# Optimization experiments

Hardware: AMD Instinct MI355X
Metric: run time of the kernel (lower is better)

The kernel has to match this reference:

```python
import jax, jax.numpy as jnp
import numpy as np

EPS = 1e-5

def conv(x, w, stride=1, pad=0):
    # x: NCHW, w: OIHW
    return jax.lax.conv_general_dilated(
        x, w, (stride, stride), [(pad, pad), (pad, pad)],
        dimension_numbers=('NCHW', 'OIHW', 'NCHW'))

def bn(x, g, b, m, v):
    scale = (g * jax.lax.rsqrt(v + EPS))[None, :, None, None]
    shift = (b - m * g * jax.lax.rsqrt(v + EPS))[None, :, None, None]
    return x * scale + shift

def dilate3x3(mask):
    # binary dilation == 3x3 max-pool, stride 1, pad 1
    return jax.lax.reduce_window(mask, -jnp.inf, jax.lax.max,
                                 (1, 1, 3, 3), (1, 1, 1, 1),
                                 [(0, 0), (0, 0), (1, 1), (1, 1)])

def setup_inputs() -> dict:
    key = jax.random.key(0)
    ks = jax.random.split(key, 8)
    B, Cin, H, W = 32, 256, 56, 56
    width, Cout = 64, 256
    f32 = jnp.float32
    return {
        'x':       jax.random.normal(ks[0], (B, Cin, H, W), f32),
        'conv1_w': jax.random.normal(ks[1], (width, Cin, 1, 1), f32) * 0.05,
        'conv2_w': jax.random.normal(ks[2], (width, width, 3, 3), f32) * 0.05,
        'conv3_w': jax.random.normal(ks[3], (Cout, width, 1, 1), f32) * 0.05,
        'bn1_g': jnp.ones((width,), f32), 'bn1_b': jnp.zeros((width,), f32),
        'bn1_m': jax.random.normal(ks[4], (width,), f32) * 0.1,
        'bn1_v': jax.random.uniform(ks[4], (width,), f32, 0.5, 1.5),
        'bn2_g': jnp.ones((width,), f32), 'bn2_b': jnp.zeros((width,), f32),
        'bn2_m': jax.random.normal(ks[5], (width,), f32) * 0.1,
        'bn2_v': jax.random.uniform(ks[5], (width,), f32, 0.5, 1.5),
        'bn3_g': jnp.ones((Cout,), f32), 'bn3_b': jnp.zeros((Cout,), f32),
        'bn3_m': jax.random.normal(ks[6], (Cout,), f32) * 0.1,
        'bn3_v': jax.random.uniform(ks[6], (Cout,), f32, 0.5, 1.5),
        'mask_w': jax.random.normal(ks[7], (1, Cin, 1, 1), f32) * 0.05,
        'mask_b': jnp.zeros((1,), f32),
    }

def reference(x, conv1_w, conv2_w, conv3_w,
              bn1_g, bn1_b, bn1_m, bn1_v,
              bn2_g, bn2_b, bn2_m, bn2_v,
              bn3_g, bn3_b, bn3_m, bn3_v,
              mask_w, mask_b):
    identity = x  # stride=1, no downsample
    # --- MaskUnit: 1x1 conv squeeze -> hard binary mask (inference Gumbel) ---
    soft = conv(x, mask_w) + mask_b[None, :, None, None]   # [B,1,H,W]
    mask = (soft >= 0.0).astype(x.dtype)                    # 'std' mask
    mask_dilate = dilate3x3(mask)                           # 'dilate' mask
    # --- sparse bottleneck: compute only on active positions (zero elsewhere) ---
    h = conv(x, conv1_w)                                    # [B,64,H,W]
    h = jax.nn.relu(bn(h, bn1_g, bn1_b, bn1_m, bn1_v)) * mask_dilate
    h = conv(h, conv2_w, stride=1, pad=1)
    h = jax.nn.relu(bn(h, bn2_g, bn2_b, bn2_m, bn2_v)) * mask
    h = conv(h, conv3_w)                                    # [B,256,H,W]
    h = bn(h, bn3_g, bn3_b, bn3_m, bn3_v) * mask            # apply_mask
    out = jax.nn.relu(identity + h)
    return out
```

## Files before the change

kernel.cpp:

```cpp
#include <hip/hip_runtime.h>
#include <hip/hip_bf16.h>


#define BATCH 32
#define CIN   256
#define WIDTH 64
#define COUT  256
#define HH    56
#define WW    56
#define HW    3136
#define EPS   1e-5f
#define XSTR  40
#define H1ROW 7424

typedef __attribute__((ext_vector_type(8))) short bf16x8;
typedef __attribute__((ext_vector_type(4))) float f32x4;

static __device__ __forceinline__ unsigned short f2bf(float f) {
    __hip_bfloat16 h = __float2bfloat16(f);
    return *reinterpret_cast<unsigned short*>(&h);
}

__global__ __launch_bounds__(384) void kbn(
    const float* __restrict__ g1, const float* __restrict__ b1,
    const float* __restrict__ m1, const float* __restrict__ v1,
    const float* __restrict__ g2, const float* __restrict__ b2,
    const float* __restrict__ m2, const float* __restrict__ v2,
    const float* __restrict__ g3, const float* __restrict__ b3,
    const float* __restrict__ m3, const float* __restrict__ v3,
    float* __restrict__ tabs)
{
    int t = threadIdx.x;
    if (t < 64) {
        float sc = g1[t] * rsqrtf(v1[t] + EPS);
        tabs[t] = sc; tabs[64 + t] = b1[t] - m1[t] * sc;
    } else if (t < 128) {
        int o = t - 64;
        float sc = g2[o] * rsqrtf(v2[o] + EPS);
        tabs[128 + o] = sc; tabs[192 + o] = b2[o] - m2[o] * sc;
    } else if (t < 384) {
        int o = t - 128;
        float sc = g3[o] * rsqrtf(v3[o] + EPS);
        tabs[256 + o] = sc; tabs[512 + o] = b3[o] - m3[o] * sc;
    }
}

__global__ __launch_bounds__(256) void kw_pack(
    const float* __restrict__ w1, const float* __restrict__ w2,
    const float* __restrict__ w3, __hip_bfloat16* __restrict__ w1p,
    __hip_bfloat16* __restrict__ w2p, __hip_bfloat16* __restrict__ w3q)
{
    int idx = blockIdx.x * 256 + threadIdx.x;
    if (idx < 16384) {
        int j = idx & 7, l = (idx >> 3) & 63;
        int mt = (idx >> 9) & 3, kt = idx >> 11;
        int o = mt * 16 + (l & 15);
        int c = kt * 32 + (l >> 4) * 8 + j;
        *reinterpret_cast<unsigned short*>(w1p + idx) = f2bf(w1[o * CIN + c]);
    } else if (idx < 16384 + 36864) {
        int i2 = idx - 16384;
        int j = i2 & 7, l = (i2 >> 3) & 63;
        int mt = (i2 >> 9) & 3, kt = (i2 >> 11) & 1, tap = i2 >> 12;
        int o = mt * 16 + (l & 15);
        int c = kt * 32 + (l >> 4) * 8 + j;
        *reinterpret_cast<unsigned short*>(w2p + i2) =
            f2bf(w2[(o * WIDTH + c) * 9 + tap]);
    } else if (idx < 16384 + 36864 + 16384) {
        int i3 = idx - 16384 - 36864;
        int j = i3 & 7, l = (i3 >> 3) & 63;
        int ot = (i3 >> 9) & 15, kt = i3 >> 13;
        int oc = ot * 16 + (l & 15);
        int c = kt * 32 + (l >> 4) * 8 + j;
        *reinterpret_cast<unsigned short*>(w3q + i3) = f2bf(w3[oc * WIDTH + c]);
    }
}

__global__ __launch_bounds__(256) void k1_mfma(
    const float* __restrict__ x, const __hip_bfloat16* __restrict__ w1p,
    const float* __restrict__ sc1, const float* __restrict__ sh1,
    const float* __restrict__ mw, const float* __restrict__ mb,
    __hip_bfloat16* __restrict__ h1g, float* __restrict__ mask)
{
    __shared__ __align__(16) unsigned short xs[2][64 * XSTR];
    __shared__ __align__(16) float mtab[16][68];

    const int tid = threadIdx.x;
    const int l = tid & 63, w = tid >> 6;
    const int ln = l & 15, lg = l >> 4;
    const int b = blockIdx.y;
    const int px0 = blockIdx.x * 64;
    const float* __restrict__ xb = x + (size_t)b * CIN * HW;
    const bf16x8* __restrict__ w1v = reinterpret_cast<const bf16x8*>(w1p);

    const int chA = tid >> 4;
    const int pxs = (tid & 15) * 4;
    float msum[4] = {0.f, 0.f, 0.f, 0.f};

    auto STAGE = [&](int kt, int bufi) {
        const float* xp = xb + (size_t)(kt * 32 + chA) * HW + px0 + pxs;
        float4 va = *reinterpret_cast<const float4*>(xp);
        float4 vb = *reinterpret_cast<const float4*>(xp + (size_t)16 * HW);
        float mwa = mw[kt * 32 + chA], mwb = mw[kt * 32 + 16 + chA];
        msum[0] += va.x * mwa + vb.x * mwb;
        msum[1] += va.y * mwa + vb.y * mwb;
        msum[2] += va.z * mwa + vb.z * mwb;
        msum[3] += va.w * mwa + vb.w * mwb;
        unsigned base = (unsigned)pxs * XSTR + chA;
        xs[bufi][base + 0 * XSTR] = f2bf(va.x);
        xs[bufi][base + 1 * XSTR] = f2bf(va.y);
        xs[bufi][base + 2 * XSTR] = f2bf(va.z);
        xs[bufi][base + 3 * XSTR] = f2bf(va.w);
        xs[bufi][base + 16 + 0 * XSTR] = f2bf(vb.x);
        xs[bufi][base + 16 + 1 * XSTR] = f2bf(vb.y);
        xs[bufi][base + 16 + 2 * XSTR] = f2bf(vb.z);
        xs[bufi][base + 16 + 3 * XSTR] = f2bf(vb.w);
    };

    f32x4 acc[4];
    #pragma unroll
    for (int m = 0; m < 4; ++m) acc[m] = f32x4{0.f, 0.f, 0.f, 0.f};

    STAGE(0, 0);
    __syncthreads();

    const unsigned fidx = (unsigned)(w * 16 + ln) * XSTR + lg * 8;
    #pragma unroll
    for (int kt = 0; kt < 8; ++kt) {
        const int cur = kt & 1;
        if (kt < 7) STAGE(kt + 1, cur ^ 1);
        bf16x8 bfr = *reinterpret_cast<const bf16x8*>(&xs[cur][fidx]);
        #pragma unroll
        for (int mt = 0; mt < 4; ++mt) {
            bf16x8 a = w1v[(kt * 4 + mt) * 64 + l];
            acc[mt] = __builtin_amdgcn_mfma_f32_16x16x32_bf16(a, bfr, acc[mt], 0, 0, 0);
        }
        __syncthreads();
    }

    *reinterpret_cast<float4*>(&mtab[chA][pxs]) =
        make_float4(msum[0], msum[1], msum[2], msum[3]);
    __syncthreads();
    if (tid < 64) {
        float s = 0.f;
        #pragma unroll
        for (int g = 0; g < 16; ++g) s += mtab[g][tid];
        mask[b * HW + px0 + tid] = (s + mb[0] >= 0.f) ? 1.f : 0.f;
    }

    const int p = px0 + w * 16 + ln;
    const int y = p / 56, xcn = p - y * 56;
    const int pxp = xcn + 1;
    const unsigned key = (unsigned)(pxp & 7) << 3;
    const size_t rowbase = (((size_t)b * 58 + y + 1) * 58 + pxp) * 64;
    #pragma unroll
    for (int mt = 0; mt < 4; ++mt) {
        int ob = mt * 16 + lg * 4;
        ushort4 u;
        u.x = f2bf(fmaxf(acc[mt][0] * sc1[ob + 0] + sh1[ob + 0], 0.f));
        u.y = f2bf(fmaxf(acc[mt][1] * sc1[ob + 1] + sh1[ob + 1], 0.f));
        u.z = f2bf(fmaxf(acc[mt][2] * sc1[ob + 2] + sh1[ob + 2], 0.f));
        u.w = f2bf(fmaxf(acc[mt][3] * sc1[ob + 3] + sh1[ob + 3], 0.f));
        *reinterpret_cast<ushort4*>(h1g + rowbase + (ob ^ key)) = u;
    }
}

__global__ __launch_bounds__(256) void k1b_dilate(
    const float* __restrict__ mask, __hip_bfloat16* __restrict__ h1g)
{
    int idx = blockIdx.x * 256 + threadIdx.x;
    if (idx >= BATCH * 58 * 58) return;
    int b   = idx / 3364;
    int rem = idx - b * 3364;
    int r = rem / 58, c = rem - r * 58;

    bool zero;
    if (r == 0 || r == 57 || c == 0 || c == 57) {
        zero = true;
    } else {
        int y = r - 1, x = c - 1;
        float mx = 0.f;
        #pragma unroll
        for (int dy = -1; dy <= 1; ++dy)
            #pragma unroll
            for (int dx = -1; dx <= 1; ++dx) {
                int yy = y + dy, xx = x + dx;
                if (yy >= 0 && yy < HH && xx >= 0 && xx < WW)
                    mx = fmaxf(mx, mask[b * HW + yy * WW + xx]);
            }
        zero = (mx < 0.5f);
    }
    if (zero) {
        uint4 z = make_uint4(0u, 0u, 0u, 0u);
        uint4* p = reinterpret_cast<uint4*>(h1g + (size_t)idx * 64);
        #pragma unroll
        for (int k = 0; k < 8; ++k) p[k] = z;
    }
}

__global__ __launch_bounds__(256) void k2_mfma(
    const __hip_bfloat16* __restrict__ h1g,
    const __hip_bfloat16* __restrict__ w2p,
    const float* __restrict__ sc2, const float* __restrict__ sh2,
    const float* __restrict__ mask, __hip_bfloat16* __restrict__ h2)
{
    __shared__ __align__(16) char smem[30720];

    const int tid = threadIdx.x;
    const int l = tid & 63, w = tid >> 6;
    const int b = blockIdx.y;
    const int yr0 = blockIdx.x * 2;
    const int yrow = yr0 + (w & 1);
    const int mh = w >> 1;
    const int ln = l & 15, lg = l >> 4;

    {
        const char* src = (const char*)h1g + ((size_t)b * 58 + yr0) * H1ROW;
        #pragma unroll
        for (int t = 0; t < 8; ++t) {
            int c = t * 4 + w;
            if (c < 29) {
                __builtin_amdgcn_global_load_lds(
                    (const __attribute__((address_space(1))) void*)(src + c * 1024 + l * 16),
                    (__attribute__((address_space(3))) void*)(smem + c * 1024),
                    16, 0, 0);
            }
        }
    }

    const bf16x8* __restrict__ w2v = reinterpret_cast<const bf16x8*>(w2p);

    f32x4 acc[2][4];
    #pragma unroll
    for (int i = 0; i < 2; ++i)
        #pragma unroll
        for (int j = 0; j < 4; ++j) acc[i][j] = f32x4{0.f, 0.f, 0.f, 0.f};

    __syncthreads();

    #pragma unroll
    for (int dy = 0; dy < 3; ++dy) {
        const int lr = (w & 1) + dy;
        #pragma unroll
        for (int dx = 0; dx < 3; ++dx) {
            const int tap = dy * 3 + dx;
            #pragma unroll
            for (int kt = 0; kt < 2; ++kt) {
                bf16x8 a0 = w2v[((tap * 2 + kt) * 4 + mh * 2 + 0) * 64 + l];
                bf16x8 a1 = w2v[((tap * 2 + kt) * 4 + mh * 2 + 1) * 64 + l];
                bf16x8 bf[4];
                #pragma unroll
                for (int nt = 0; nt < 4; ++nt) {
                    int colp = nt * 16 + ln + dx;
                    unsigned off = (unsigned)lr * H1ROW + (unsigned)colp * 128
                                 + (((unsigned)(kt * 64 + lg * 16))
                                    ^ (((unsigned)colp & 7u) << 4));
                    bf[nt] = *reinterpret_cast<const bf16x8*>(smem + off);
                }
                #pragma unroll
                for (int nt = 0; nt < 4; ++nt) {
                    acc[0][nt] = __builtin_amdgcn_mfma_f32_16x16x32_bf16(
                        a0, bf[nt], acc[0][nt], 0, 0, 0);
                    acc[1][nt] = __builtin_amdgcn_mfma_f32_16x16x32_bf16(
                        a1, bf[nt], acc[1][nt], 0, 0, 0);
                }
            }
        }
    }

    #pragma unroll
    for (int nt = 0; nt < 4; ++nt) {
        int xc = nt * 16 + ln;
        if (xc < WW) {
            int p = yrow * WW + xc;
            float mkv = mask[b * HW + p];
            #pragma unroll
            for (int mi = 0; mi < 2; ++mi) {
                int ob = (mh * 2 + mi) * 16 + lg * 4;
                ushort4 u;
                u.x = f2bf(fmaxf(acc[mi][nt][0] * sc2[ob + 0] + sh2[ob + 0], 0.f) * mkv);
                u.y = f2bf(fmaxf(acc[mi][nt][1] * sc2[ob + 1] + sh2[ob + 1], 0.f) * mkv);
                u.z = f2bf(fmaxf(acc[mi][nt][2] * sc2[ob + 2] + sh2[ob + 2], 0.f) * mkv);
                u.w = f2bf(fmaxf(acc[mi][nt][3] * sc2[ob + 3] + sh2[ob + 3], 0.f) * mkv);
                *reinterpret_cast<ushort4*>(h2 + ((size_t)b * HW + p) * 64 + ob) = u;
            }
        }
    }
}

__global__ __launch_bounds__(256) void k3_mfma(
    const __hip_bfloat16* __restrict__ h2, const __hip_bfloat16* __restrict__ w3q,
    const float* __restrict__ sc3, const float* __restrict__ sh3,
    const float* __restrict__ x, const float* __restrict__ mask,
    float* __restrict__ out)
{
    const int tid = threadIdx.x;
    const int l = tid & 63, w = tid >> 6;
    const int ln = l & 15, lg = l >> 4;
    const int b = blockIdx.y;
    const int yr = blockIdx.x;

    const bf16x8* __restrict__ h2v = reinterpret_cast<const bf16x8*>(h2)
                                   + ((size_t)b * HW + yr * WW) * 8;
    const bf16x8* __restrict__ w3v = reinterpret_cast<const bf16x8*>(w3q);

    float4 mk4[4];
    #pragma unroll
    for (int pt = 0; pt < 4; ++pt) {
        int pxb = pt * 16 + lg * 4;
        mk4[pt] = (pxb < WW)
            ? *reinterpret_cast<const float4*>(&mask[(size_t)b * HW + yr * WW + pxb])
            : make_float4(0.f, 0.f, 0.f, 0.f);
    }
    float4 xv[4][4];
    #pragma unroll
    for (int ot = 0; ot < 4; ++ot) {
        const int oc = w * 64 + ot * 16 + ln;
        const size_t rbase = ((size_t)b * COUT + oc) * HW + yr * WW;
        #pragma unroll
        for (int pt = 0; pt < 4; ++pt) {
            int pxb = pt * 16 + lg * 4;
            if (pxb < WW)
                xv[ot][pt] = *reinterpret_cast<const float4*>(&x[rbase + pxb]);
        }
    }

    f32x4 acc[4][4];
    #pragma unroll
    for (int p = 0; p < 4; ++p)
        #pragma unroll
        for (int o = 0; o < 4; ++o) acc[p][o] = f32x4{0.f, 0.f, 0.f, 0.f};

    #pragma unroll
    for (int kt = 0; kt < 2; ++kt) {
        bf16x8 af[4];
        #pragma unroll
        for (int pt = 0; pt < 4; ++pt)
            af[pt] = h2v[(pt * 16 + ln) * 8 + kt * 4 + lg];
        #pragma unroll
        for (int ot = 0; ot < 4; ++ot) {
            bf16x8 bw = w3v[(kt * 16 + w * 4 + ot) * 64 + l];
            #pragma unroll
            for (int pt = 0; pt < 4; ++pt)
                acc[pt][ot] = __builtin_amdgcn_mfma_f32_16x16x32_bf16(
                    af[pt], bw, acc[pt][ot], 0, 0, 0);
        }
    }

    #pragma unroll
    for (int ot = 0; ot < 4; ++ot) {
        const int oc = w * 64 + ot * 16 + ln;
        const float sc = sc3[oc], sh = sh3[oc];
        const size_t rbase = ((size_t)b * COUT + oc) * HW + yr * WW;
        #pragma unroll
        for (int pt = 0; pt < 4; ++pt) {
            int pxb = pt * 16 + lg * 4;
            if (pxb < WW) {
                float4 o4;
                o4.x = fmaxf(xv[ot][pt].x + (acc[pt][ot][0] * sc + sh) * mk4[pt].x, 0.f);
                o4.y = fmaxf(xv[ot][pt].y + (acc[pt][ot][1] * sc + sh) * mk4[pt].y, 0.f);
                o4.z = fmaxf(xv[ot][pt].z + (acc[pt][ot][2] * sc + sh) * mk4[pt].z, 0.f);
                o4.w = fmaxf(xv[ot][pt].w + (acc[pt][ot][3] * sc + sh) * mk4[pt].w, 0.f);
                *reinterpret_cast<float4*>(&out[rbase + pxb]) = o4;
            }
        }
    }
}

extern "C" void kernel_launch(void* const* d_in, const int* in_sizes, int n_in,
                              void* d_out, int out_size, void* d_ws, size_t ws_size,
                              hipStream_t stream)
{
    const float* x  = (const float*)d_in[0];
    const float* w1 = (const float*)d_in[1];
    const float* w2 = (const float*)d_in[2];
    const float* w3 = (const float*)d_in[3];
    const float* g1 = (const float*)d_in[4];
    const float* b1 = (const float*)d_in[5];
    const float* m1 = (const float*)d_in[6];
    const float* v1 = (const float*)d_in[7];
    const float* g2 = (const float*)d_in[8];
    const float* b2 = (const float*)d_in[9];
    const float* m2 = (const float*)d_in[10];
    const float* v2 = (const float*)d_in[11];
    const float* g3 = (const float*)d_in[12];
    const float* b3 = (const float*)d_in[13];
    const float* m3 = (const float*)d_in[14];
    const float* v3 = (const float*)d_in[15];
    const float* mw = (const float*)d_in[16];
    const float* mb = (const float*)d_in[17];
    float* outp = (float*)d_out;

    char* p = (char*)d_ws;
    __hip_bfloat16* h1g = (__hip_bfloat16*)p;  p += (size_t)BATCH * 3364 * 64 * 2;
    __hip_bfloat16* h2  = (__hip_bfloat16*)p;  p += (size_t)BATCH * HW * 64 * 2;
    float* mask = (float*)p;                   p += (size_t)BATCH * HW * 4;
    __hip_bfloat16* w1p = (__hip_bfloat16*)p;  p += 16384 * 2;
    __hip_bfloat16* w2p = (__hip_bfloat16*)p;  p += 36864 * 2;
    __hip_bfloat16* w3q = (__hip_bfloat16*)p;  p += 16384 * 2;
    float* tabs = (float*)p;
    float* sc1 = tabs;       float* sh1 = tabs + 64;
    float* sc2 = tabs + 128; float* sh2 = tabs + 192;
    float* sc3 = tabs + 256; float* sh3 = tabs + 512;

    kbn<<<dim3(1), dim3(384), 0, stream>>>(g1, b1, m1, v1, g2, b2, m2, v2,
                                           g3, b3, m3, v3, tabs);
    kw_pack<<<dim3(272), dim3(256), 0, stream>>>(w1, w2, w3, w1p, w2p, w3q);

    k1_mfma<<<dim3(49, BATCH), dim3(256), 0, stream>>>(x, w1p, sc1, sh1, mw, mb,
                                                       h1g, mask);

    int npad = BATCH * 3364;
    k1b_dilate<<<dim3((npad + 255) / 256), dim3(256), 0, stream>>>(mask, h1g);

    k2_mfma<<<dim3(HH / 2, BATCH), dim3(256), 0, stream>>>(h1g, w2p, sc2, sh2,
                                                           mask, h2);

    k3_mfma<<<dim3(HH, BATCH), dim3(256), 0, stream>>>(h2, w3q, sc3, sh3,
                                                       x, mask, outp);
}
```

Before: 102.1 us.

## Fuse dilated-mask zeroing into conv2 smem tile, merge BN prep, split conv3 channels

The separate dilation kernel, which zeroed inactive and border positions of h1 in global memory, is removed. Instead, k2 computes the 3x3 max of the mask for each staged pixel and zeroes those pixels directly in its shared-memory tile after the async load. The BN-table kernel is folded into the weight-packing kernel as an extra block, saving one launch. k3 now splits output channels across a new grid z dimension of 2 to raise parallelism and cut per-thread accumulators, at the cost of reading h2 twice.

```diff
diff --git a/kernel.cpp b/kernel.cpp
--- a/kernel.cpp
+++ b/kernel.cpp
@@ -21,7 +21,10 @@
     return *reinterpret_cast<unsigned short*>(&h);
 }
 
-__global__ __launch_bounds__(384) void kbn(
+__global__ __launch_bounds__(256) void kw_pack(
+    const float* __restrict__ w1, const float* __restrict__ w2,
+    const float* __restrict__ w3, __hip_bfloat16* __restrict__ w1p,
+    __hip_bfloat16* __restrict__ w2p, __hip_bfloat16* __restrict__ w3q,
     const float* __restrict__ g1, const float* __restrict__ b1,
     const float* __restrict__ m1, const float* __restrict__ v1,
     const float* __restrict__ g2, const float* __restrict__ b2,
@@ -30,26 +33,23 @@
     const float* __restrict__ m3, const float* __restrict__ v3,
     float* __restrict__ tabs)
 {
-    int t = threadIdx.x;
-    if (t < 64) {
-        float sc = g1[t] * rsqrtf(v1[t] + EPS);
-        tabs[t] = sc; tabs[64 + t] = b1[t] - m1[t] * sc;
-    } else if (t < 128) {
-        int o = t - 64;
-        float sc = g2[o] * rsqrtf(v2[o] + EPS);
-        tabs[128 + o] = sc; tabs[192 + o] = b2[o] - m2[o] * sc;
-    } else if (t < 384) {
-        int o = t - 128;
-        float sc = g3[o] * rsqrtf(v3[o] + EPS);
-        tabs[256 + o] = sc; tabs[512 + o] = b3[o] - m3[o] * sc;
-    }
-}
-
-__global__ __launch_bounds__(256) void kw_pack(
-    const float* __restrict__ w1, const float* __restrict__ w2,
-    const float* __restrict__ w3, __hip_bfloat16* __restrict__ w1p,
-    __hip_bfloat16* __restrict__ w2p, __hip_bfloat16* __restrict__ w3q)
-{
+    if (blockIdx.x == 272) {
+        for (int t = threadIdx.x; t < 384; t += 256) {
+            if (t < 64) {
+                float sc = g1[t] * rsqrtf(v1[t] + EPS);
+                tabs[t] = sc; tabs[64 + t] = b1[t] - m1[t] * sc;
+            } else if (t < 128) {
+                int o = t - 64;
+                float sc = g2[o] * rsqrtf(v2[o] + EPS);
+                tabs[128 + o] = sc; tabs[192 + o] = b2[o] - m2[o] * sc;
+            } else {
+                int o = t - 128;
+                float sc = g3[o] * rsqrtf(v3[o] + EPS);
+                tabs[256 + o] = sc; tabs[512 + o] = b3[o] - m3[o] * sc;
+            }
+        }
+        return;
+    }
     int idx = blockIdx.x * 256 + threadIdx.x;
     if (idx < 16384) {
         int j = idx & 7, l = (idx >> 3) & 63;
@@ -164,39 +164,6 @@
     }
 }
 
-__global__ __launch_bounds__(256) void k1b_dilate(
-    const float* __restrict__ mask, __hip_bfloat16* __restrict__ h1g)
-{
-    int idx = blockIdx.x * 256 + threadIdx.x;
-    if (idx >= BATCH * 58 * 58) return;
-    int b   = idx / 3364;
-    int rem = idx - b * 3364;
-    int r = rem / 58, c = rem - r * 58;
-
-    bool zero;
-    if (r == 0 || r == 57 || c == 0 || c == 57) {
-        zero = true;
-    } else {
-        int y = r - 1, x = c - 1;
-        float mx = 0.f;
-        #pragma unroll
-        for (int dy = -1; dy <= 1; ++dy)
-            #pragma unroll
-            for (int dx = -1; dx <= 1; ++dx) {
-                int yy = y + dy, xx = x + dx;
-                if (yy >= 0 && yy < HH && xx >= 0 && xx < WW)
-                    mx = fmaxf(mx, mask[b * HW + yy * WW + xx]);
-            }
-        zero = (mx < 0.5f);
-    }
-    if (zero) {
-        uint4 z = make_uint4(0u, 0u, 0u, 0u);
-        uint4* p = reinterpret_cast<uint4*>(h1g + (size_t)idx * 64);
-        #pragma unroll
-        for (int k = 0; k < 8; ++k) p[k] = z;
-    }
-}
-
 __global__ __launch_bounds__(256) void k2_mfma(
     const __hip_bfloat16* __restrict__ h1g,
     const __hip_bfloat16* __restrict__ w2p,
@@ -235,6 +202,35 @@
         #pragma unroll
         for (int j = 0; j < 4; ++j) acc[i][j] = f32x4{0.f, 0.f, 0.f, 0.f};
 
+    __syncthreads();
+
+    if (tid < 232) {
+        const int pr = tid / 58;
+        const int pc = tid - pr * 58;
+        const int gr = yr0 + pr;
+        bool zero;
+        if (gr == 0 || gr == 57 || pc == 0 || pc == 57) {
+            zero = true;
+        } else {
+            const int y = gr - 1, xc = pc - 1;
+            float mx = 0.f;
+            #pragma unroll
+            for (int dy = -1; dy <= 1; ++dy)
+                #pragma unroll
+                for (int dx = -1; dx <= 1; ++dx) {
+                    int yy = y + dy, xx = xc + dx;
+                    if (yy >= 0 && yy < HH && xx >= 0 && xx < WW)
+                        mx = fmaxf(mx, mask[b * HW + yy * WW + xx]);
+                }
+            zero = (mx < 0.5f);
+        }
+        if (zero) {
+            uint4* q = reinterpret_cast<uint4*>(smem + pr * H1ROW + pc * 128);
+            uint4 zz = make_uint4(0u, 0u, 0u, 0u);
+            #pragma unroll
+            for (int k = 0; k < 8; ++k) q[k] = zz;
+        }
+    }
     __syncthreads();
 
     #pragma unroll
@@ -298,6 +294,7 @@
     const int ln = l & 15, lg = l >> 4;
     const int b = blockIdx.y;
     const int yr = blockIdx.x;
+    const int z = blockIdx.z;
 
     const bf16x8* __restrict__ h2v = reinterpret_cast<const bf16x8*>(h2)
                                    + ((size_t)b * HW + yr * WW) * 8;
@@ -311,10 +308,10 @@
             ? *reinterpret_cast<const float4*>(&mask[(size_t)b * HW + yr * WW + pxb])
             : make_float4(0.f, 0.f, 0.f, 0.f);
     }
-    float4 xv[4][4];
-    #pragma unroll
-    for (int ot = 0; ot < 4; ++ot) {
-        const int oc = w * 64 + ot * 16 + ln;
+    float4 xv[2][4];
+    #pragma unroll
+    for (int ot = 0; ot < 2; ++ot) {
+        const int oc = w * 64 + z * 32 + ot * 16 + ln;
         const size_t rbase = ((size_t)b * COUT + oc) * HW + yr * WW;
         #pragma unroll
         for (int pt = 0; pt < 4; ++pt) {
@@ -324,11 +321,11 @@
         }
     }
 
-    f32x4 acc[4][4];
+    f32x4 acc[4][2];
     #pragma unroll
     for (int p = 0; p < 4; ++p)
         #pragma unroll
-        for (int o = 0; o < 4; ++o) acc[p][o] = f32x4{0.f, 0.f, 0.f, 0.f};
+        for (int o = 0; o < 2; ++o) acc[p][o] = f32x4{0.f, 0.f, 0.f, 0.f};
 
     #pragma unroll
     for (int kt = 0; kt < 2; ++kt) {
@@ -337,8 +334,8 @@
         for (int pt = 0; pt < 4; ++pt)
             af[pt] = h2v[(pt * 16 + ln) * 8 + kt * 4 + lg];
         #pragma unroll
-        for (int ot = 0; ot < 4; ++ot) {
-            bf16x8 bw = w3v[(kt * 16 + w * 4 + ot) * 64 + l];
+        for (int ot = 0; ot < 2; ++ot) {
+            bf16x8 bw = w3v[(kt * 16 + w * 4 + z * 2 + ot) * 64 + l];
             #pragma unroll
             for (int pt = 0; pt < 4; ++pt)
                 acc[pt][ot] = __builtin_amdgcn_mfma_f32_16x16x32_bf16(
@@ -347,8 +344,8 @@
     }
 
     #pragma unroll
-    for (int ot = 0; ot < 4; ++ot) {
-        const int oc = w * 64 + ot * 16 + ln;
+    for (int ot = 0; ot < 2; ++ot) {
+        const int oc = w * 64 + z * 32 + ot * 16 + ln;
         const float sc = sc3[oc], sh = sh3[oc];
         const size_t rbase = ((size_t)b * COUT + oc) * HW + yr * WW;
         #pragma unroll
@@ -402,19 +399,16 @@
     float* sc2 = tabs + 128; float* sh2 = tabs + 192;
     float* sc3 = tabs + 256; float* sh3 = tabs + 512;
 
-    kbn<<<dim3(1), dim3(384), 0, stream>>>(g1, b1, m1, v1, g2, b2, m2, v2,
-                                           g3, b3, m3, v3, tabs);
-    kw_pack<<<dim3(272), dim3(256), 0, stream>>>(w1, w2, w3, w1p, w2p, w3q);
+    kw_pack<<<dim3(273), dim3(256), 0, stream>>>(w1, w2, w3, w1p, w2p, w3q,
+                                                 g1, b1, m1, v1, g2, b2, m2, v2,
+                                                 g3, b3, m3, v3, tabs);
 
     k1_mfma<<<dim3(49, BATCH), dim3(256), 0, stream>>>(x, w1p, sc1, sh1, mw, mb,
                                                        h1g, mask);
 
-    int npad = BATCH * 3364;
-    k1b_dilate<<<dim3((npad + 255) / 256), dim3(256), 0, stream>>>(mask, h1g);
-
     k2_mfma<<<dim3(HH / 2, BATCH), dim3(256), 0, stream>>>(h1g, w2p, sc2, sh2,
                                                            mask, h2);
 
-    k3_mfma<<<dim3(HH, BATCH), dim3(256), 0, stream>>>(h2, w3q, sc3, sh3,
-                                                       x, mask, outp);
-}
+    k3_mfma<<<dim3(HH, BATCH, 2), dim3(256), 0, stream>>>(h2, w3q, sc3, sh3,
+                                                          x, mask, outp);
+}
```

Result: faster. 98.75 us (-3.3%).
